# Kernel tuning notes

Measured on AMD Instinct MI355X. Metric: run time of the kernel, lower is better.

The kernel has to match this reference:

```python
import jax, jax.numpy as jnp
import numpy as np

Q = 128


def _maxpool2(x):
    # 2x2 max pool, stride 2, NCHW
    return jax.lax.reduce_window(x, -jnp.inf, jax.lax.max,
                                 (1, 1, 2, 2), (1, 1, 2, 2), 'VALID')


def _conv(x, w, b):
    y = jax.lax.conv_general_dilated(x, w, window_strides=(1, 1), padding='VALID',
                                     dimension_numbers=('NCHW', 'OIHW', 'NCHW'))
    return y + b[None, :, None, None]


def setup_inputs() -> dict:
    key = jax.random.key(0)
    ks = jax.random.split(key, 16)
    B = 4096
    x = jax.random.normal(ks[0], (B, 1, 28, 28), dtype=jnp.float32)
    hash_idx1 = jax.random.randint(ks[1], (25,), 0, Q, dtype=jnp.int32)
    hash_idx2 = jax.random.randint(ks[2], (800,), 0, Q, dtype=jnp.int32)
    hash_idx3 = jax.random.randint(ks[3], (1024,), 0, Q, dtype=jnp.int32)
    # random +/-1 signs
    sgn1 = jnp.sign(jax.random.normal(ks[4], (25,), dtype=jnp.float32))
    sgn2 = jnp.sign(jax.random.normal(ks[5], (800,), dtype=jnp.float32))
    sgn3 = jnp.sign(jax.random.normal(ks[6], (1024,), dtype=jnp.float32))
    # compressed (sketched) parameters: one length-Q vector per output unit
    w1 = jax.random.normal(ks[7], (32, Q), dtype=jnp.float32) * 0.2
    b1 = jax.random.normal(ks[8], (32,), dtype=jnp.float32) * 0.05
    w2 = jax.random.normal(ks[9], (64, Q), dtype=jnp.float32) * 0.05
    b2 = jax.random.normal(ks[10], (64,), dtype=jnp.float32) * 0.05
    w3 = jax.random.normal(ks[11], (512, Q), dtype=jnp.float32) * 0.03
    b3 = jax.random.normal(ks[12], (512,), dtype=jnp.float32) * 0.05
    fc2_w = jax.random.normal(ks[13], (10, 512), dtype=jnp.float32) * 0.04
    fc2_b = jax.random.normal(ks[14], (10,), dtype=jnp.float32) * 0.05
    return {'x': x,
            'hash_idx1': hash_idx1, 'hash_idx2': hash_idx2, 'hash_idx3': hash_idx3,
            'sgn1': sgn1, 'sgn2': sgn2, 'sgn3': sgn3,
            'w1': w1, 'b1': b1, 'w2': w2, 'b2': b2, 'w3': w3, 'b3': b3,
            'fc2_w': fc2_w, 'fc2_b': fc2_b}


def reference(x, hash_idx1, hash_idx2, hash_idx3, sgn1, sgn2, sgn3,
              w1, b1, w2, b2, w3, b3, fc2_w, fc2_b):
    # SketchConv1: reconstruct dense weight via gather + sign flip
    wc1 = (w1[:, hash_idx1] * sgn1[None, :]).reshape(32, 1, 5, 5)
    h = jax.nn.relu(_maxpool2(_conv(x, wc1, b1)))          # (B,32,12,12)
    # SketchConv2
    wc2 = (w2[:, hash_idx2] * sgn2[None, :]).reshape(64, 32, 5, 5)
    h = jax.nn.relu(_maxpool2(_conv(h, wc2, b2)))          # (B,64,4,4)
    h = h.reshape(h.shape[0], -1)                          # (B,1024)
    # SketchLinear
    W3 = w3[:, hash_idx3] * sgn3[None, :]                  # (512,1024)
    h = jax.nn.relu(h @ W3.T + b3)                         # (B,512)
    logits = h @ fc2_w.T + fc2_b                           # (B,10)
    return jax.nn.log_softmax(logits, axis=1)
```

## Files before the change

### kernel.cpp

```cpp
#include <hip/hip_runtime.h>
#include <hip/hip_bf16.h>
#include <math.h>


typedef __attribute__((ext_vector_type(8))) short bf16x8;
typedef __attribute__((ext_vector_type(4))) float f32x4;

static __device__ inline ushort f2bfu(float v) {
    union { __hip_bfloat16 h; ushort u; } cv;
    cv.h = __float2bfloat16(v);
    return cv.u;
}

static __device__ inline float bfu2f(ushort u) {
    union { ushort u; __hip_bfloat16 h; } cv;
    cv.u = u;
    return __bfloat162float(cv.h);
}


__global__ __launch_bounds__(256)
void k_reconstruct(const float* __restrict__ w1, const float* __restrict__ w2,
                   const float* __restrict__ w3,
                   const int* __restrict__ hi1, const int* __restrict__ hi2,
                   const int* __restrict__ hi3,
                   const float* __restrict__ s1, const float* __restrict__ s2,
                   const float* __restrict__ s3,
                   __hip_bfloat16* __restrict__ wc1f,
                   __hip_bfloat16* __restrict__ wc1s,
                   __hip_bfloat16* __restrict__ wc2f,
                   __hip_bfloat16* __restrict__ W3d,
                   int* __restrict__ cnt, uint* __restrict__ tab) {
    if (blockIdx.x == 232) {
        const int u = threadIdx.x;
        if (u < 128) cnt[u] = 0;
        __syncthreads();
        #pragma unroll
        for (int j = 0; j < 4; ++j) {
            int k = u * 4 + j;
            int q = hi3[k];
            int p = atomicAdd(&cnt[q], 1);
            if (p < 32)
                tab[q * 32 + p] = (uint)k | ((uint)f2bfu(s3[k]) << 16);
        }
        return;
    }
    const int t = blockIdx.x * blockDim.x + threadIdx.x;
    const int f = t >> 2;
    const int j0 = (t & 3) * 2;
    if (f < 256) {
        const bool shifted = f >= 128;
        const int u = f & 127;
        const int nt = u >> 6, lane = u & 63;
        const int quad = lane >> 4, l15 = lane & 15;
        const int oc = nt * 16 + l15;
        ushort rr[2];
        #pragma unroll
        for (int jj = 0; jj < 2; ++jj) {
            int tt = quad * 8 + j0 + jj;
            int ki = (tt * 43) >> 8;
            int kj = tt - 6 * ki;
            float v = 0.f;
            if (!shifted && ki < 5 && kj < 5) {
                int fi = ki * 5 + kj;
                v = w1[oc * 128 + hi1[fi]] * s1[fi];
            } else if (shifted && ki < 5 && kj >= 1 && kj <= 5) {
                int fi = ki * 5 + (kj - 1);
                v = w1[oc * 128 + hi1[fi]] * s1[fi];
            }
            rr[jj] = f2bfu(v);
        }
        *(uint*)((ushort*)(shifted ? wc1s : wc1f) + (size_t)u * 8 + j0) =
            (uint)rr[0] | ((uint)rr[1] << 16);
    } else if (f < 6656) {
        const int u = f - 256;
        const int l15 = u & 15, quad = (u >> 4) & 3;
        const int ntA = (u >> 6) & 3, tap = u >> 8;
        const int oc = ntA * 16 + l15;
        ushort rr[2];
        #pragma unroll
        for (int jj = 0; jj < 2; ++jj) {
            int ic = quad * 8 + j0 + jj;
            int fi = ic * 25 + tap;
            rr[jj] = f2bfu(w2[oc * 128 + hi2[fi]] * s2[fi]);
        }
        *(uint*)((ushort*)wc2f + (size_t)u * 8 + j0) =
            (uint)rr[0] | ((uint)rr[1] << 16);
    } else if (f < 14848) {
        const int u = f - 6656;
        const int l15 = u & 15, quad = (u >> 4) & 3;
        const int kt = (u >> 6) & 3, ntile = u >> 8;
        const int n = ntile * 16 + l15;
        ushort rr[2];
        #pragma unroll
        for (int jj = 0; jj < 2; ++jj) {
            int k = kt * 32 + quad * 8 + j0 + jj;
            rr[jj] = f2bfu(w3[n * 128 + k]);
        }
        *(uint*)((ushort*)W3d + (size_t)u * 8 + j0) =
            (uint)rr[0] | ((uint)rr[1] << 16);
    }
}

__global__ __launch_bounds__(512, 6)
void k_conv(const float* __restrict__ x,
            const __hip_bfloat16* __restrict__ wc1f,
            const __hip_bfloat16* __restrict__ wc1s,
            const __hip_bfloat16* __restrict__ wc2f,
            const float* __restrict__ b1, const float* __restrict__ b2,
            __hip_bfloat16* __restrict__ h2) {
    __shared__ __align__(16) ushort s_xb[4 * 816];
    __shared__ __align__(16) ushort s_h1[16 * 1160];

    const int tid = threadIdx.x;
    const int b0 = blockIdx.x * 4;
    const int wave = tid >> 6, lane = tid & 63;
    const int l15 = lane & 15, quad = lane >> 4;

    {
        const float4* xg = (const float4*)(x + (size_t)b0 * 784);
        for (int i = tid; i < 784; i += 512) {
            float4 v = xg[i];
            int img = i / 196;
            int pos = (i - img * 196) * 4;
            ushort* dst = &s_xb[img * 816 + pos];
            dst[0] = f2bfu(v.x); dst[1] = f2bfu(v.y);
            dst[2] = f2bfu(v.z); dst[3] = f2bfu(v.w);
        }
        if (tid < 128) {
            int img = tid >> 5, k = tid & 31;
            s_xb[img * 816 + 784 + k] = 0;
        }
    }

    bf16x8 bw1[2], bw1s[2];
    float bb1[2];
    #pragma unroll
    for (int nt = 0; nt < 2; ++nt) {
        bw1[nt]  = *(const bf16x8*)((const ushort*)wc1f + (nt * 64 + lane) * 8);
        bw1s[nt] = *(const bf16x8*)((const ushort*)wc1s + (nt * 64 + lane) * 8);
        bb1[nt] = b1[nt * 16 + l15];
    }
    __syncthreads();

    {
        const int img = wave >> 1, half = wave & 1;
        const int sub = l15 & 3;
        const ushort* srcImg = s_xb + img * 816;
        int offr[4];
        #pragma unroll
        for (int r = 0; r < 4; ++r) {
            int t = quad * 8 + 2 * r;
            int row = (t * 43) >> 8;
            int col = t - 6 * row;
            offr[r] = row * 28 + col;
        }
        const int g0 = l15 >> 3, r0 = l15 & 7;
        #pragma unroll
        for (int ii = 0; ii < 18; ++ii) {
            const int i = half * 18 + ii;
            const int pb = 4 * i + (l15 >> 2);
            const int pi = (pb * 171) >> 11;
            const int pj = pb - 12 * pi;
            const int base_e = (2 * pi + (sub >> 1)) * 28 + 2 * pj;
            const ushort* p0 = srcImg + base_e;
            union { bf16x8 v; uint u[4]; } A;
            A.u[0] = *(const uint*)(p0 + offr[0]);
            A.u[1] = *(const uint*)(p0 + offr[1]);
            A.u[2] = *(const uint*)(p0 + offr[2]);
            A.u[3] = *(const uint*)(p0 + offr[3]);
            f32x4 z = {0.f, 0.f, 0.f, 0.f};
            f32x4 ce0 = __builtin_amdgcn_mfma_f32_16x16x32_bf16(A.v, bw1[0],  z, 0, 0, 0);
            f32x4 co0 = __builtin_amdgcn_mfma_f32_16x16x32_bf16(A.v, bw1s[0], z, 0, 0, 0);
            f32x4 ce1 = __builtin_amdgcn_mfma_f32_16x16x32_bf16(A.v, bw1[1],  z, 0, 0, 0);
            f32x4 co1 = __builtin_amdgcn_mfma_f32_16x16x32_bf16(A.v, bw1s[1], z, 0, 0, 0);
            const int pbo = 4 * i + quad;
            float m0 = fmaxf(fmaxf(ce0[0], co0[1]), fmaxf(ce0[2], co0[3]));
            float m1 = fmaxf(fmaxf(ce1[0], co1[1]), fmaxf(ce1[2], co1[3]));
            s_h1[(img * 4 + g0) * 1160 + pbo * 8 + r0]     = f2bfu(fmaxf(m0 + bb1[0], 0.f));
            s_h1[(img * 4 + 2 + g0) * 1160 + pbo * 8 + r0] = f2bfu(fmaxf(m1 + bb1[1], 0.f));
        }
    }
    __syncthreads();

    const int pr = wave >> 1, nh = wave & 1;
    const int sub2 = l15 & 3;
    const int ci2 = 2 * pr + (sub2 >> 1);
    const int cj2 = 2 * (l15 >> 2) + (sub2 & 1);
    const int posBase = (ci2 * 12 + cj2) * 8;

    f32x4 acc[4][2];
    float bb2[2];
    #pragma unroll
    for (int ntl = 0; ntl < 2; ++ntl) {
        bb2[ntl] = b2[(nh * 2 + ntl) * 16 + l15];
        #pragma unroll
        for (int img = 0; img < 4; ++img)
            acc[img][ntl] = (f32x4){0.f, 0.f, 0.f, 0.f};
    }

    #pragma unroll
    for (int tap = 0; tap < 25; ++tap) {
        const int ki = tap / 5, kj = tap % 5;
        const int off = (ki * 12 + kj) * 8;
        bf16x8 a[4];
        #pragma unroll
        for (int img = 0; img < 4; ++img)
            a[img] = *(const bf16x8*)&s_h1[(img * 4 + quad) * 1160 + posBase + off];
        #pragma unroll
        for (int ntl = 0; ntl < 2; ++ntl) {
            bf16x8 bf = *(const bf16x8*)((const ushort*)wc2f +
                          ((tap * 4 + nh * 2 + ntl) * 64 + lane) * 8);
            #pragma unroll
            for (int img = 0; img < 4; ++img)
                acc[img][ntl] = __builtin_amdgcn_mfma_f32_16x16x32_bf16(
                    a[img], bf, acc[img][ntl], 0, 0, 0);
        }
    }

    #pragma unroll
    for (int img = 0; img < 4; ++img)
        #pragma unroll
        for (int ntl = 0; ntl < 2; ++ntl) {
            f32x4 c = acc[img][ntl];
            float m = fmaxf(fmaxf(c[0], c[1]), fmaxf(c[2], c[3]));
            float v = fmaxf(m + bb2[ntl], 0.f);
            h2[(size_t)(b0 + img) * 1024 + ((nh * 2 + ntl) * 16 + l15) * 16 + pr * 4 + quad] =
                __float2bfloat16(v);
        }
}

__global__ __launch_bounds__(1024)
void k_fc(const __hip_bfloat16* __restrict__ A, const __hip_bfloat16* __restrict__ W3d,
          const int* __restrict__ cnt, const uint* __restrict__ tab,
          const float* __restrict__ b3, const float* __restrict__ fc2w,
          const float* __restrict__ fc2b, float* __restrict__ out) {
    __shared__ __align__(16) ushort s_A[16 * 1032];
    __shared__ __align__(16) ushort s_Ab[16 * 136];
    __shared__ float s_h3[16 * 516];

    const int tid = threadIdx.x;
    const int wave = tid >> 6, lane = tid & 63;
    const int l15 = lane & 15, quad = lane >> 4;
    const int mBase = blockIdx.x * 16;

    {
        const uint4* g = (const uint4*)(A + (size_t)(mBase + wave) * 1024);
        uint4 v0 = g[lane * 2], v1 = g[lane * 2 + 1];
        uint4* d = (uint4*)&s_A[wave * 1032 + lane * 16];
        d[0] = v0; d[1] = v1;
    }
    __syncthreads();

    {
        const ushort* arow = &s_A[wave * 1032];
        uint pack[2];
        #pragma unroll
        for (int hh = 0; hh < 2; ++hh) {
            int q = lane * 2 + hh;
            int n = cnt[q];
            float v = 0.f;
            for (int i = 0; i < n; ++i) {
                uint e = tab[q * 32 + i];
                v += bfu2f(arow[e & 0xffff]) * bfu2f((ushort)(e >> 16));
            }
            pack[hh] = f2bfu(v);
        }
        *(uint*)&s_Ab[wave * 136 + lane * 2] = pack[0] | (pack[1] << 16);
    }
    __syncthreads();

    f32x4 acc[2];
    acc[0] = (f32x4){0.f, 0.f, 0.f, 0.f};
    acc[1] = (f32x4){0.f, 0.f, 0.f, 0.f};

    const ushort* aP = &s_Ab[l15 * 136 + quad * 8];
    const ushort* bP0 = (const ushort*)W3d + ((size_t)(wave * 2)     * 4 * 64 + lane) * 8;
    const ushort* bP1 = (const ushort*)W3d + ((size_t)(wave * 2 + 1) * 4 * 64 + lane) * 8;
    #pragma unroll
    for (int kt = 0; kt < 4; ++kt) {
        bf16x8 a = *(const bf16x8*)(aP + kt * 32);
        bf16x8 bf0 = *(const bf16x8*)(bP0 + kt * 512);
        bf16x8 bf1 = *(const bf16x8*)(bP1 + kt * 512);
        acc[0] = __builtin_amdgcn_mfma_f32_16x16x32_bf16(a, bf0, acc[0], 0, 0, 0);
        acc[1] = __builtin_amdgcn_mfma_f32_16x16x32_bf16(a, bf1, acc[1], 0, 0, 0);
    }

    #pragma unroll
    for (int ntl = 0; ntl < 2; ++ntl) {
        int col = wave * 32 + ntl * 16 + l15;
        float bb = b3[col];
        #pragma unroll
        for (int r = 0; r < 4; ++r)
            s_h3[(quad * 4 + r) * 516 + col] = fmaxf(acc[ntl][r] + bb, 0.f);
    }
    __syncthreads();

    const float* hrow = &s_h3[wave * 516];
    float4 h0 = *(const float4*)&hrow[lane * 8];
    float4 h1 = *(const float4*)&hrow[lane * 8 + 4];
    float lg[10];
    #pragma unroll
    for (int c = 0; c < 10; ++c) {
        float4 w0 = *(const float4*)&fc2w[c * 512 + lane * 8];
        float4 w1 = *(const float4*)&fc2w[c * 512 + lane * 8 + 4];
        float s = h0.x * w0.x + h0.y * w0.y + h0.z * w0.z + h0.w * w0.w
                + h1.x * w1.x + h1.y * w1.y + h1.z * w1.z + h1.w * w1.w;
        s += __shfl_down(s, 32);
        s += __shfl_down(s, 16);
        s += __shfl_down(s, 8);
        s += __shfl_down(s, 4);
        s += __shfl_down(s, 2);
        s += __shfl_down(s, 1);
        lg[c] = s;
    }
    if (lane == 0) {
        float mx = -1e30f;
        #pragma unroll
        for (int c = 0; c < 10; ++c) { lg[c] += fc2b[c]; mx = fmaxf(mx, lg[c]); }
        float sum = 0.f;
        #pragma unroll
        for (int c = 0; c < 10; ++c) sum += expf(lg[c] - mx);
        float lse = mx + logf(sum);
        #pragma unroll
        for (int c = 0; c < 10; ++c)
            out[(size_t)(mBase + wave) * 10 + c] = lg[c] - lse;
    }
}

extern "C" void kernel_launch(void* const* d_in, const int* in_sizes, int n_in,
                              void* d_out, int out_size, void* d_ws, size_t ws_size,
                              hipStream_t stream) {
    const float* x    = (const float*)d_in[0];
    const int*   hi1  = (const int*)d_in[1];
    const int*   hi2  = (const int*)d_in[2];
    const int*   hi3  = (const int*)d_in[3];
    const float* s1   = (const float*)d_in[4];
    const float* s2   = (const float*)d_in[5];
    const float* s3   = (const float*)d_in[6];
    const float* w1   = (const float*)d_in[7];
    const float* b1   = (const float*)d_in[8];
    const float* w2   = (const float*)d_in[9];
    const float* b2   = (const float*)d_in[10];
    const float* w3   = (const float*)d_in[11];
    const float* b3   = (const float*)d_in[12];
    const float* fc2w = (const float*)d_in[13];
    const float* fc2b = (const float*)d_in[14];
    float* out = (float*)d_out;

    const int B = in_sizes[0] / 784;

    char* ws = (char*)d_ws;
    __hip_bfloat16* wc1f = (__hip_bfloat16*)(ws + 0);
    __hip_bfloat16* wc1s = (__hip_bfloat16*)(ws + 2048);
    __hip_bfloat16* wc2f = (__hip_bfloat16*)(ws + 4096);
    __hip_bfloat16* W3d  = (__hip_bfloat16*)(ws + 106496);
    int*            cnt  = (int*)(ws + 237568);
    uint*           tab  = (uint*)(ws + 238080);
    __hip_bfloat16* h2   = (__hip_bfloat16*)(ws + 1155072);

    k_reconstruct<<<233, 256, 0, stream>>>(
        w1, w2, w3, hi1, hi2, hi3, s1, s2, s3, wc1f, wc1s, wc2f, W3d, cnt, tab);
    k_conv<<<B / 4, 512, 0, stream>>>(x, wc1f, wc1s, wc2f, b1, b2, h2);
    k_fc<<<B / 16, 1024, 0, stream>>>(h2, W3d, cnt, tab, b3, fc2w, fc2b, out);
}
```

Before: 141.3 us.

## Permute conv2 output by hash bucket so FC sketch sums contiguous segments

The reconstruct kernel now builds a counting-sort permutation of the 1024 flattened features by hash bucket (shared-memory atomics plus a prefix scan), producing segment offsets and per-feature positions. The conv kernel writes each pooled activation pre-multiplied by its sign into its permuted slot. The FC kernel then sums contiguous LDS ranges per bucket instead of chasing an index/sign table from global memory. This removes the dependent table loads and the 32-per-bucket cap in the FC gather, at the cost of scattered global stores in the conv epilogue.

Measured after the change: 135.7 us. 4.0% less time.

```diff
diff --git a/kernel.cpp b/kernel.cpp
--- a/kernel.cpp
+++ b/kernel.cpp
@@ -25,24 +25,48 @@
                    const int* __restrict__ hi1, const int* __restrict__ hi2,
                    const int* __restrict__ hi3,
                    const float* __restrict__ s1, const float* __restrict__ s2,
-                   const float* __restrict__ s3,
                    __hip_bfloat16* __restrict__ wc1f,
                    __hip_bfloat16* __restrict__ wc1s,
                    __hip_bfloat16* __restrict__ wc2f,
                    __hip_bfloat16* __restrict__ W3d,
-                   int* __restrict__ cnt, uint* __restrict__ tab) {
+                   int* __restrict__ seg, int* __restrict__ pos) {
     if (blockIdx.x == 232) {
+        __shared__ int scnt[128];
+        __shared__ int sincl[128];
+        __shared__ int sseg[129];
         const int u = threadIdx.x;
-        if (u < 128) cnt[u] = 0;
+        if (u < 128) scnt[u] = 0;
         __syncthreads();
+        int qq[4], rk[4];
         #pragma unroll
         for (int j = 0; j < 4; ++j) {
             int k = u * 4 + j;
-            int q = hi3[k];
-            int p = atomicAdd(&cnt[q], 1);
-            if (p < 32)
-                tab[q * 32 + p] = (uint)k | ((uint)f2bfu(s3[k]) << 16);
-        }
+            qq[j] = hi3[k];
+            rk[j] = atomicAdd(&scnt[qq[j]], 1);
+        }
+        __syncthreads();
+        if (u < 128) {
+            int v = scnt[u];
+            #pragma unroll
+            for (int d = 1; d < 64; d <<= 1) {
+                int t2 = __shfl_up(v, d);
+                if ((u & 63) >= d) v += t2;
+            }
+            sincl[u] = v;
+        }
+        __syncthreads();
+        if (u < 128) {
+            int base = (u >= 64) ? sincl[63] : 0;
+            sseg[u + 1] = base + sincl[u];
+        }
+        if (u == 0) sseg[0] = 0;
+        __syncthreads();
+        #pragma unroll
+        for (int j = 0; j < 4; ++j) {
+            int k = u * 4 + j;
+            pos[k] = sseg[qq[j]] + rk[j];
+        }
+        if (u < 129) seg[u] = sseg[u];
         return;
     }
     const int t = blockIdx.x * blockDim.x + threadIdx.x;
@@ -108,6 +132,7 @@
             const __hip_bfloat16* __restrict__ wc1s,
             const __hip_bfloat16* __restrict__ wc2f,
             const float* __restrict__ b1, const float* __restrict__ b2,
+            const int* __restrict__ pos, const float* __restrict__ s3,
             __hip_bfloat16* __restrict__ h2) {
     __shared__ __align__(16) ushort s_xb[4 * 816];
     __shared__ __align__(16) ushort s_h1[16 * 1160];
@@ -122,8 +147,8 @@
         for (int i = tid; i < 784; i += 512) {
             float4 v = xg[i];
             int img = i / 196;
-            int pos = (i - img * 196) * 4;
-            ushort* dst = &s_xb[img * 816 + pos];
+            int p = (i - img * 196) * 4;
+            ushort* dst = &s_xb[img * 816 + p];
             dst[0] = f2bfu(v.x); dst[1] = f2bfu(v.y);
             dst[2] = f2bfu(v.z); dst[3] = f2bfu(v.w);
         }
@@ -218,32 +243,39 @@
         }
     }
 
-    #pragma unroll
-    for (int img = 0; img < 4; ++img)
-        #pragma unroll
-        for (int ntl = 0; ntl < 2; ++ntl) {
-            f32x4 c = acc[img][ntl];
-            float m = fmaxf(fmaxf(c[0], c[1]), fmaxf(c[2], c[3]));
-            float v = fmaxf(m + bb2[ntl], 0.f);
-            h2[(size_t)(b0 + img) * 1024 + ((nh * 2 + ntl) * 16 + l15) * 16 + pr * 4 + quad] =
-                __float2bfloat16(v);
-        }
+    const int k0 = ((nh * 2 + 0) * 16 + l15) * 16 + pr * 4 + quad;
+    const int k1 = ((nh * 2 + 1) * 16 + l15) * 16 + pr * 4 + quad;
+    const int p0 = pos[k0], p1 = pos[k1];
+    const float sg0 = s3[k0], sg1 = s3[k1];
+    #pragma unroll
+    for (int img = 0; img < 4; ++img) {
+        f32x4 c0 = acc[img][0];
+        float m0 = fmaxf(fmaxf(c0[0], c0[1]), fmaxf(c0[2], c0[3]));
+        float v0 = fmaxf(m0 + bb2[0], 0.f);
+        h2[(size_t)(b0 + img) * 1024 + p0] = __float2bfloat16(v0 * sg0);
+        f32x4 c1 = acc[img][1];
+        float m1 = fmaxf(fmaxf(c1[0], c1[1]), fmaxf(c1[2], c1[3]));
+        float v1 = fmaxf(m1 + bb2[1], 0.f);
+        h2[(size_t)(b0 + img) * 1024 + p1] = __float2bfloat16(v1 * sg1);
+    }
 }
 
 __global__ __launch_bounds__(1024)
 void k_fc(const __hip_bfloat16* __restrict__ A, const __hip_bfloat16* __restrict__ W3d,
-          const int* __restrict__ cnt, const uint* __restrict__ tab,
+          const int* __restrict__ seg,
           const float* __restrict__ b3, const float* __restrict__ fc2w,
           const float* __restrict__ fc2b, float* __restrict__ out) {
     __shared__ __align__(16) ushort s_A[16 * 1032];
     __shared__ __align__(16) ushort s_Ab[16 * 136];
     __shared__ float s_h3[16 * 516];
+    __shared__ int s_seg[132];
 
     const int tid = threadIdx.x;
     const int wave = tid >> 6, lane = tid & 63;
     const int l15 = lane & 15, quad = lane >> 4;
     const int mBase = blockIdx.x * 16;
 
+    if (tid < 129) s_seg[tid] = seg[tid];
     {
         const uint4* g = (const uint4*)(A + (size_t)(mBase + wave) * 1024);
         uint4 v0 = g[lane * 2], v1 = g[lane * 2 + 1];
@@ -254,19 +286,17 @@
 
     {
         const ushort* arow = &s_A[wave * 1032];
-        uint pack[2];
-        #pragma unroll
-        for (int hh = 0; hh < 2; ++hh) {
-            int q = lane * 2 + hh;
-            int n = cnt[q];
-            float v = 0.f;
-            for (int i = 0; i < n; ++i) {
-                uint e = tab[q * 32 + i];
-                v += bfu2f(arow[e & 0xffff]) * bfu2f((ushort)(e >> 16));
-            }
-            pack[hh] = f2bfu(v);
-        }
-        *(uint*)&s_Ab[wave * 136 + lane * 2] = pack[0] | (pack[1] << 16);
+        const int q0 = lane * 2;
+        const int a0 = s_seg[q0], e0 = s_seg[q0 + 1], e1 = s_seg[q0 + 2];
+        const int n0 = e0 - a0, n1 = e1 - e0;
+        const int nm = max(n0, n1);
+        float v0 = 0.f, v1 = 0.f;
+        for (int i = 0; i < nm; ++i) {
+            if (i < n0) v0 += bfu2f(arow[a0 + i]);
+            if (i < n1) v1 += bfu2f(arow[e0 + i]);
+        }
+        *(uint*)&s_Ab[wave * 136 + lane * 2] =
+            (uint)f2bfu(v0) | ((uint)f2bfu(v1) << 16);
     }
     __syncthreads();
 
@@ -355,12 +385,12 @@
     __hip_bfloat16* wc1s = (__hip_bfloat16*)(ws + 2048);
     __hip_bfloat16* wc2f = (__hip_bfloat16*)(ws + 4096);
     __hip_bfloat16* W3d  = (__hip_bfloat16*)(ws + 106496);
-    int*            cnt  = (int*)(ws + 237568);
-    uint*           tab  = (uint*)(ws + 238080);
+    int*            seg  = (int*)(ws + 237568);
+    int*            pos  = (int*)(ws + 238592);
     __hip_bfloat16* h2   = (__hip_bfloat16*)(ws + 1155072);
 
     k_reconstruct<<<233, 256, 0, stream>>>(
-        w1, w2, w3, hi1, hi2, hi3, s1, s2, s3, wc1f, wc1s, wc2f, W3d, cnt, tab);
-    k_conv<<<B / 4, 512, 0, stream>>>(x, wc1f, wc1s, wc2f, b1, b2, h2);
-    k_fc<<<B / 16, 1024, 0, stream>>>(h2, W3d, cnt, tab, b3, fc2w, fc2b, out);
-}
+        w1, w2, w3, hi1, hi2, hi3, s1, s2, wc1f, wc1s, wc2f, W3d, seg, pos);
+    k_conv<<<B / 4, 512, 0, stream>>>(x, wc1f, wc1s, wc2f, b1, b2, pos, s3, h2);
+    k_fc<<<B / 16, 1024, 0, stream>>>(h2, W3d, seg, b3, fc2w, fc2b, out);
+}
```
